# Performance work log

Hardware: AMD Instinct MI355X
Metric: run time of the kernel (lower is better)

Reference implementation:

```python
import jax, jax.numpy as jnp
import numpy as np

D_MODEL = 512
D_INNER = 2 * D_MODEL      # 1024
DT_RANK = D_MODEL // 16    # 32
D_STATE = 16
D_CONV = 4
NB_LAYERS = 3
BATCH = 64
SEQ = 201
CITY = 200
EPS = 1e-5


def setup_inputs() -> dict:
    key = jax.random.key(0)
    ks = jax.random.split(key, 12)
    def rn(k, shape, scale=0.02):
        return jax.random.normal(k, shape, jnp.float32) * scale
    A_init = jnp.tile(jnp.arange(1, D_STATE + 1, dtype=jnp.float32)[None, None, :],
                      (NB_LAYERS, D_INNER, 1))
    return {
        "x": jax.random.uniform(ks[0], (BATCH, SEQ, 2), jnp.float32),
        "city_count": CITY,
        "embed_W": rn(ks[1], (D_MODEL, 2), 0.5),
        "embed_b": jnp.zeros((D_MODEL,), jnp.float32),
        "norm_w": jnp.ones((NB_LAYERS, D_MODEL), jnp.float32),
        "norm_b": jnp.zeros((NB_LAYERS, D_MODEL), jnp.float32),
        "in_W": rn(ks[2], (NB_LAYERS, 2 * D_INNER, D_MODEL)),
        "conv_w": rn(ks[3], (NB_LAYERS, D_INNER, D_CONV), 0.1),
        "conv_b": jnp.zeros((NB_LAYERS, D_INNER), jnp.float32),
        "xproj_W": rn(ks[4], (NB_LAYERS, DT_RANK + 2 * D_STATE, D_INNER)),
        "dtproj_W": rn(ks[5], (NB_LAYERS, D_INNER, DT_RANK), 0.1),
        "dtproj_b": rn(ks[6], (NB_LAYERS, D_INNER), 0.5),
        "A_log": jnp.log(A_init),
        "Dskip": jnp.ones((NB_LAYERS, D_INNER), jnp.float32),
        "out_W": rn(ks[7], (NB_LAYERS, D_MODEL, D_INNER)),
        "normf_w": jnp.ones((D_MODEL,), jnp.float32),
        "normf_b": jnp.zeros((D_MODEL,), jnp.float32),
        "head_W": rn(ks[8], (CITY, D_MODEL)),
    }


def _silu(v):
    return v * jax.nn.sigmoid(v)


def _layernorm(v, w, b):
    v = v.astype(jnp.float32)
    mu = v.mean(-1, keepdims=True)
    var = ((v - mu) ** 2).mean(-1, keepdims=True)
    return (v - mu) * jax.lax.rsqrt(var + EPS) * w + b


def _rmsnorm(v, w, b):
    v = v.astype(jnp.float32)
    ms = (v * v).mean(-1, keepdims=True)
    return v * jax.lax.rsqrt(ms + EPS) * w + b


def _mamba_mixer(h, in_W, cw, cb, xp_W, dt_W, dt_b, A_log, Dv, o_W):
    B, L, _ = h.shape
    xz = jnp.einsum('bld,ed->ble', h, in_W)              # (B,L,2*di)
    xc, z = jnp.split(xz, 2, axis=-1)
    # causal depthwise conv over time
    xt = xc.transpose(0, 2, 1)                           # (B,di,L)
    xt = jax.lax.conv_general_dilated(
        xt, cw[:, None, :], (1,), [(D_CONV - 1, 0)],
        dimension_numbers=('NCH', 'OIH', 'NCH'),
        feature_group_count=D_INNER)
    u = _silu((xt + cb[None, :, None]).transpose(0, 2, 1))   # (B,L,di)
    x_dbl = jnp.einsum('bld,ed->ble', u, xp_W)
    dt_r = x_dbl[..., :DT_RANK]
    Bm = x_dbl[..., DT_RANK:DT_RANK + D_STATE]
    Cm = x_dbl[..., DT_RANK + D_STATE:]
    dt = jax.nn.softplus(jnp.einsum('blr,dr->bld', dt_r, dt_W) + dt_b)
    A = -jnp.exp(A_log)                                  # (di,n)

    def step(hst, ins):
        dt_t, B_t, C_t, u_t = ins                        # (B,di),(B,n),(B,n),(B,di)
        dA = jnp.exp(dt_t[..., None] * A)                # (B,di,n)
        hst = dA * hst + (dt_t * u_t)[..., None] * B_t[:, None, :]
        y = jnp.einsum('bdn,bn->bd', hst, C_t)
        return hst, y

    h0 = jnp.zeros((B, D_INNER, D_STATE), h.dtype)
    _, ys = jax.lax.scan(step, h0, (dt.transpose(1, 0, 2), Bm.transpose(1, 0, 2),
                                    Cm.transpose(1, 0, 2), u.transpose(1, 0, 2)))
    y = ys.transpose(1, 0, 2) + Dv * u
    y = y * _silu(z)
    return jnp.einsum('bld,ed->ble', y, o_W)


def reference(x, city_count, embed_W, embed_b, norm_w, norm_b, in_W, conv_w, conv_b,
              xproj_W, dtproj_W, dtproj_b, A_log, Dskip, out_W, normf_w, normf_b, head_W):
    h = jnp.einsum('blc,dc->bld', x, embed_W) + embed_b
    residual = None
    for i in range(NB_LAYERS):
        residual = h if residual is None else h + residual   # residual in fp32
        hn = _layernorm(residual, norm_w[i], norm_b[i])
        h = _mamba_mixer(hn, in_W[i], conv_w[i], conv_b[i], xproj_W[i],
                         dtproj_W[i], dtproj_b[i], A_log[i], Dskip[i], out_W[i])
    residual = h + residual
    xf = _rmsnorm(residual, normf_w, normf_b)                # final fused RMSNorm
    logits = jnp.einsum('bld,cd->blc', xf, head_W)           # output head -> city logits
    return logits
```

## Files before the change

kernel.cpp:

```cpp
#include <hip/hip_runtime.h>
#include <hip/hip_fp16.h>
#include <math.h>

#define D_MODEL 512
#define D_INNER 1024
#define DT_RANK 32
#define D_STATE 16
#define D_CONV 4
#define NB_LAYERS 3
#define BATCH 64
#define SEQ 201
#define CITY 200
#define M_ROWS (BATCH * SEQ)
#define M_PAD 12928
#define EPS 1e-5f
#define NCH 8
#define CL 26

typedef __attribute__((ext_vector_type(8))) short short8;
typedef __attribute__((ext_vector_type(8))) unsigned short ushort8;
typedef __attribute__((ext_vector_type(4))) float f32x4;

__device__ __forceinline__ float sigmoidf_(float x) { return 1.f / (1.f + __expf(-x)); }

__device__ __forceinline__ unsigned short f2b(float f) {
  union { float f; unsigned int u; } v; v.f = f;
  unsigned int r = (v.u + 0x7fff + ((v.u >> 16) & 1)) >> 16;
  return (unsigned short)r;
}
__device__ __forceinline__ float b2f(unsigned short h) {
  union { unsigned int u; float f; } v; v.u = ((unsigned int)h) << 16; return v.f;
}
__device__ __forceinline__ unsigned short f2h(float f) {
  __half h = __float2half(f); return *(unsigned short*)&h;
}
__device__ __forceinline__ float h2f(unsigned short u) {
  __half h = *(__half*)&u; return __half2float(h);
}

__device__ __forceinline__ void gload_lds16(const void* g, void* l) {
  __builtin_amdgcn_global_load_lds(
      (const __attribute__((address_space(1))) void*)g,
      (__attribute__((address_space(3))) void*)l, 16, 0, 0);
}

__device__ __forceinline__ void exp_vec(float dtv, const float* __restrict__ Areg,
                                        bool fast, float* __restrict__ e) {
  if (fast) {
    float e1 = __expf(-dtv);
    e[0] = e1;
    e[1] = e1 * e1;
    e[2] = e[1] * e1;
    e[3] = e[1] * e[1];
    e[4] = e[3] * e1;
    e[5] = e[3] * e[1];
    e[6] = e[3] * e[2];
    e[7] = e[3] * e[3];
    e[8] = e[7] * e1;
    e[9] = e[7] * e[1];
    e[10] = e[7] * e[2];
    e[11] = e[7] * e[3];
    e[12] = e[7] * e[4];
    e[13] = e[7] * e[5];
    e[14] = e[7] * e[6];
    e[15] = e[7] * e[7];
  } else {
#pragma unroll
    for (int n = 0; n < D_STATE; ++n) e[n] = __expf(dtv * Areg[n]);
  }
}
__device__ __forceinline__ bool a_is_arange(const float* __restrict__ Areg) {
  bool f = true;
#pragma unroll
  for (int n = 0; n < D_STATE; ++n)
    f = f && (fabsf(Areg[n] + (float)(n + 1)) < 1e-4f * (float)(n + 1));
  return f;
}

__global__ __launch_bounds__(256) void k_f2b(const float* __restrict__ in,
                                             unsigned short* __restrict__ out,
                                             int n, int n_total) {
  int i = blockIdx.x * 256 + threadIdx.x;
  if (i < n) out[i] = f2b(in[i]);
  else if (i < n_total) out[i] = 0;
}

__global__ __launch_bounds__(256) void k_padR(const float* __restrict__ W,
                                              unsigned short* __restrict__ out,
                                              int nl, int inrows, int outrows, int cols) {
  int i = blockIdx.x * 256 + threadIdx.x;
  if (i >= nl * outrows * cols) return;
  int c = i % cols;
  int r = (i / cols) % outrows;
  int L = i / (cols * outrows);
  out[i] = (r < inrows) ? f2b(W[((size_t)L * inrows + r) * cols + c]) : 0;
}

__global__ __launch_bounds__(256) void k_convT(const float* __restrict__ cw,
                                               float* __restrict__ cwT) {
  int i = blockIdx.x * 256 + threadIdx.x;
  if (i >= NB_LAYERS * D_CONV * D_INNER) return;
  int d = i & (D_INNER - 1);
  int k = (i >> 10) & 3;
  int L = i >> 12;
  cwT[i] = cw[((size_t)L * D_INNER + d) * D_CONV + k];
}

__global__ __launch_bounds__(256) void k_embed(const float* __restrict__ x,
                                               const float* __restrict__ W,
                                               const float* __restrict__ b,
                                               float* __restrict__ h) {
  int idx = blockIdx.x * 256 + threadIdx.x;
  if (idx >= M_ROWS * D_MODEL) return;
  int d = idx & (D_MODEL - 1);
  int m = idx >> 9;
  float x0 = x[m * 2 + 0], x1 = x[m * 2 + 1];
  h[idx] = fmaf(x0, W[d * 2 + 0], fmaf(x1, W[d * 2 + 1], b[d]));
}

__global__ __launch_bounds__(256) void k_resid_norm(const float* __restrict__ h,
                                                    float* __restrict__ resid,
                                                    float* __restrict__ out,
                                                    unsigned short* __restrict__ out_b,
                                                    const float* __restrict__ w,
                                                    const float* __restrict__ b,
                                                    int addRes, int mode) {
  int row = blockIdx.x * 4 + (threadIdx.x >> 6);
  int lane = threadIdx.x & 63;
  if (row >= M_ROWS) return;
  const float* hp = h + (size_t)row * D_MODEL;
  float* rp = resid + (size_t)row * D_MODEL;
  float v[8];
#pragma unroll
  for (int j = 0; j < 8; ++j) {
    float t = hp[j * 64 + lane];
    if (addRes) t += rp[j * 64 + lane];
    v[j] = t;
    rp[j * 64 + lane] = t;
  }
  float mu = 0.f, rstd;
  if (mode == 0) {
    float s = 0.f;
#pragma unroll
    for (int j = 0; j < 8; ++j) s += v[j];
#pragma unroll
    for (int o = 1; o < 64; o <<= 1) s += __shfl_xor(s, o);
    mu = s * (1.f / D_MODEL);
    float vs = 0.f;
#pragma unroll
    for (int j = 0; j < 8; ++j) { float d0 = v[j] - mu; vs += d0 * d0; }
#pragma unroll
    for (int o = 1; o < 64; o <<= 1) vs += __shfl_xor(vs, o);
    rstd = rsqrtf(vs * (1.f / D_MODEL) + EPS);
  } else {
    float s = 0.f;
#pragma unroll
    for (int j = 0; j < 8; ++j) s += v[j] * v[j];
#pragma unroll
    for (int o = 1; o < 64; o <<= 1) s += __shfl_xor(s, o);
    rstd = rsqrtf(s * (1.f / D_MODEL) + EPS);
  }
#pragma unroll
  for (int j = 0; j < 8; ++j) {
    int c = j * 64 + lane;
    float o = (v[j] - mu) * rstd * w[c] + b[c];
    if (out) out[(size_t)row * D_MODEL + c] = o;
    if (out_b) out_b[(size_t)row * D_MODEL + c] = f2b(o);
  }
}

template <int BOUT>
__global__ __launch_bounds__(256) void k_gemm_mfma(const unsigned short* __restrict__ A,
                                                   const unsigned short* __restrict__ B,
                                                   void* __restrict__ Cv, int ldc,
                                                   int M, int Nout, int K) {
  __shared__ unsigned short lA[128 * 64];
  __shared__ unsigned short lB[128 * 64];
  int tid = threadIdx.x;
  int wave = tid >> 6, lane = tid & 63;
  int nx = gridDim.x;
  int nwg = nx * gridDim.y;
  int bid = blockIdx.y * nx + blockIdx.x;
  int q = nwg >> 3, rr = nwg & 7;
  int xcd = bid & 7, idx = bid >> 3;
  int swz = (xcd < rr ? xcd * (q + 1) : rr * (q + 1) + (xcd - rr) * q) + idx;
  int bm = (swz / nx) * 128, bn = (swz % nx) * 128;
  int wm = (wave >> 1) * 64, wn = (wave & 1) * 64;
  f32x4 acc[4][4] = {};

  for (int k0 = 0; k0 < K; k0 += 64) {
#pragma unroll
    for (int i = 0; i < 4; ++i) {
      int e = (i * 256 + tid) * 8;
      int r = e >> 6, c = e & 63;
      int csrc = c ^ ((r & 7) << 3);
      gload_lds16(A + (size_t)(bm + r) * K + k0 + csrc, &lA[e]);
      gload_lds16(B + (size_t)(bn + r) * K + k0 + csrc, &lB[e]);
    }
    __syncthreads();
#pragma unroll
    for (int ks = 0; ks < 2; ++ks) {
      int koff = ks * 32 + (lane >> 4) * 8;
      short8 a[4], b[4];
#pragma unroll
      for (int i = 0; i < 4; ++i) {
        int row = wm + i * 16 + (lane & 15);
        a[i] = *(const short8*)&lA[row * 64 + (koff ^ ((row & 7) << 3))];
      }
#pragma unroll
      for (int j = 0; j < 4; ++j) {
        int row = wn + j * 16 + (lane & 15);
        b[j] = *(const short8*)&lB[row * 64 + (koff ^ ((row & 7) << 3))];
      }
#pragma unroll
      for (int i = 0; i < 4; ++i)
#pragma unroll
        for (int j = 0; j < 4; ++j)
          acc[i][j] = __builtin_amdgcn_mfma_f32_16x16x32_bf16(a[i], b[j], acc[i][j], 0, 0, 0);
    }
    __syncthreads();
  }
#pragma unroll
  for (int i = 0; i < 4; ++i) {
    int row0 = bm + wm + i * 16 + (lane >> 4) * 4;
#pragma unroll
    for (int j = 0; j < 4; ++j) {
      int col = bn + wn + j * 16 + (lane & 15);
#pragma unroll
      for (int r = 0; r < 4; ++r) {
        int m = row0 + r;
        if (m < M && col < Nout) {
          float v = acc[i][j][r];
          if (BOUT == 1) ((unsigned short*)Cv)[(size_t)m * ldc + col] = f2b(v);
          else ((float*)Cv)[(size_t)m * ldc + col] = v;
        }
      }
    }
  }
}

__global__ __launch_bounds__(256) void k_conv_silu(const unsigned short* __restrict__ xz,
                                                   const float* __restrict__ cwT,
                                                   const float* __restrict__ cb,
                                                   unsigned short* __restrict__ ub) {
  int i = blockIdx.x * 256 + threadIdx.x;
  if (i >= M_ROWS * 128) return;
  int dg = (i & 127) << 3;
  int m = i >> 7;
  int l = m % SEQ;
  float y[8];
  float4 cb0 = *(const float4*)&cb[dg];
  float4 cb1 = *(const float4*)&cb[dg + 4];
  y[0] = cb0.x; y[1] = cb0.y; y[2] = cb0.z; y[3] = cb0.w;
  y[4] = cb1.x; y[5] = cb1.y; y[6] = cb1.z; y[7] = cb1.w;
#pragma unroll
  for (int k = 0; k < D_CONV; ++k) {
    int ls = l - (D_CONV - 1) + k;
    if (ls >= 0) {
      ushort8 xv = *(const ushort8*)&xz[(size_t)(m - (D_CONV - 1) + k) * 2048 + dg];
      float4 w0 = *(const float4*)&cwT[k * D_INNER + dg];
      float4 w1 = *(const float4*)&cwT[k * D_INNER + dg + 4];
      y[0] = fmaf(w0.x, b2f(xv[0]), y[0]);
      y[1] = fmaf(w0.y, b2f(xv[1]), y[1]);
      y[2] = fmaf(w0.z, b2f(xv[2]), y[2]);
      y[3] = fmaf(w0.w, b2f(xv[3]), y[3]);
      y[4] = fmaf(w1.x, b2f(xv[4]), y[4]);
      y[5] = fmaf(w1.y, b2f(xv[5]), y[5]);
      y[6] = fmaf(w1.z, b2f(xv[6]), y[6]);
      y[7] = fmaf(w1.w, b2f(xv[7]), y[7]);
    }
  }
  ushort8 o;
#pragma unroll
  for (int j = 0; j < 8; ++j) { float v = y[j]; v = v * sigmoidf_(v); o[j] = f2b(v); }
  *(ushort8*)&ub[(size_t)m * D_INNER + dg] = o;
}

__device__ __forceinline__ float dt_eval(const float* __restrict__ xq,
                                         const float* __restrict__ Wd, float bias) {
  float a0 = 0.f, a1 = 0.f, a2 = 0.f, a3 = 0.f;
#pragma unroll
  for (int r = 0; r < 2; ++r) {
    float4 q0 = *(const float4*)&xq[r * 16 + 0];
    float4 q1 = *(const float4*)&xq[r * 16 + 4];
    float4 q2 = *(const float4*)&xq[r * 16 + 8];
    float4 q3 = *(const float4*)&xq[r * 16 + 12];
    int o = r * 16;
    a0 = fmaf(q0.x, Wd[o + 0], a0); a0 = fmaf(q0.y, Wd[o + 1], a0);
    a0 = fmaf(q0.z, Wd[o + 2], a0); a0 = fmaf(q0.w, Wd[o + 3], a0);
    a1 = fmaf(q1.x, Wd[o + 4], a1); a1 = fmaf(q1.y, Wd[o + 5], a1);
    a1 = fmaf(q1.z, Wd[o + 6], a1); a1 = fmaf(q1.w, Wd[o + 7], a1);
    a2 = fmaf(q2.x, Wd[o + 8], a2); a2 = fmaf(q2.y, Wd[o + 9], a2);
    a2 = fmaf(q2.z, Wd[o + 10], a2); a2 = fmaf(q2.w, Wd[o + 11], a2);
    a3 = fmaf(q3.x, Wd[o + 12], a3); a3 = fmaf(q3.y, Wd[o + 13], a3);
    a3 = fmaf(q3.z, Wd[o + 14], a3); a3 = fmaf(q3.w, Wd[o + 15], a3);
  }
  float dot = ((a0 + a1) + (a2 + a3)) + bias;
  return (dot > 20.f) ? dot : __logf(1.f + __expf(dot));
}

__global__ __launch_bounds__(256) void k_scan_p1(const unsigned short* __restrict__ ub,
                                                 const float* __restrict__ xdb,
                                                 const float* __restrict__ dtW,
                                                 const float* __restrict__ dtb,
                                                 const float* __restrict__ A_log,
                                                 unsigned short* __restrict__ dt,
                                                 unsigned short* __restrict__ L,
                                                 float* __restrict__ dtsum) {
  int tid = threadIdx.x;
  int b = blockIdx.x >> 3, c = blockIdx.x & 7;
  int d = blockIdx.y * 256 + tid;
  int t0 = c * CL, t1 = t0 + CL < SEQ ? t0 + CL : SEQ;
  float Wd[DT_RANK];
#pragma unroll
  for (int r = 0; r < DT_RANK; r += 4) {
    float4 w4 = *(const float4*)&dtW[(size_t)d * DT_RANK + r];
    Wd[r] = w4.x; Wd[r + 1] = w4.y; Wd[r + 2] = w4.z; Wd[r + 3] = w4.w;
  }
  float bias = dtb[d];
  float Areg[D_STATE], hst[D_STATE];
#pragma unroll
  for (int n = 0; n < D_STATE; ++n) {
    Areg[n] = -__expf(A_log[d * D_STATE + n]);
    hst[n] = 0.f;
  }
  bool fast = a_is_arange(Areg);
  float ds = 0.f;
  size_t row0 = (size_t)b * SEQ;
  for (int t = t0; t < t1; ++t) {
    size_t m = row0 + t;
    const float* xq = xdb + m * 64;
    unsigned short dh = f2h(dt_eval(xq, Wd, bias));
    dt[m * D_INNER + d] = dh;
    float dtv = h2f(dh);
    float uv = b2f(ub[m * D_INNER + d]);
    float Bv[D_STATE];
#pragma unroll
    for (int qd = 0; qd < 4; ++qd) {
      float4 v4 = *(const float4*)&xq[32 + qd * 4];
      Bv[qd * 4 + 0] = v4.x; Bv[qd * 4 + 1] = v4.y;
      Bv[qd * 4 + 2] = v4.z; Bv[qd * 4 + 3] = v4.w;
    }
    float du = dtv * uv;
    ds += dtv;
    float e[D_STATE];
    exp_vec(dtv, Areg, fast, e);
#pragma unroll
    for (int j = 0; j < D_STATE; ++j)
      hst[j] = fmaf(e[j], hst[j], du * Bv[j]);
  }
  size_t base = ((size_t)(b * NCH + c) * D_INNER + d) * D_STATE;
  ushort8 o0, o1;
#pragma unroll
  for (int j = 0; j < 8; ++j) { o0[j] = f2b(hst[j]); o1[j] = f2b(hst[8 + j]); }
  *(ushort8*)&L[base] = o0;
  *(ushort8*)&L[base + 8] = o1;
  dtsum[(size_t)(b * NCH + c) * D_INNER + d] = ds;
}

__global__ __launch_bounds__(256) void k_scan_fix(const float* __restrict__ A_log,
                                                  const float* __restrict__ dtsum,
                                                  unsigned short* __restrict__ L) {
  int tid = threadIdx.x;
  int b = blockIdx.x;
  int d = blockIdx.y * 256 + tid;
  float Areg[D_STATE], h[D_STATE];
#pragma unroll
  for (int n = 0; n < D_STATE; ++n) {
    Areg[n] = -__expf(A_log[d * D_STATE + n]);
    h[n] = 0.f;
  }
  bool fast = a_is_arange(Areg);
  for (int c = 0; c < NCH; ++c) {
    size_t base = ((size_t)(b * NCH + c) * D_INNER + d) * D_STATE;
    ushort8 l0 = *(const ushort8*)&L[base];
    ushort8 l1 = *(const ushort8*)&L[base + 8];
    float ds = dtsum[(size_t)(b * NCH + c) * D_INNER + d];
    ushort8 o0, o1;
#pragma unroll
    for (int j = 0; j < 8; ++j) { o0[j] = f2b(h[j]); o1[j] = f2b(h[8 + j]); }
    *(ushort8*)&L[base] = o0;
    *(ushort8*)&L[base + 8] = o1;
    float e[D_STATE];
    exp_vec(ds, Areg, fast, e);
#pragma unroll
    for (int j = 0; j < 8; ++j)
      h[j] = fmaf(e[j], h[j], b2f(l0[j]));
#pragma unroll
    for (int j = 0; j < 8; ++j)
      h[8 + j] = fmaf(e[8 + j], h[8 + j], b2f(l1[j]));
  }
}

__global__ __launch_bounds__(256) void k_scan_p2(const unsigned short* __restrict__ xz,
                                                 const unsigned short* __restrict__ ub,
                                                 const float* __restrict__ xdb,
                                                 const unsigned short* __restrict__ dt,
                                                 const float* __restrict__ A_log,
                                                 const float* __restrict__ Dv,
                                                 const unsigned short* __restrict__ L,
                                                 unsigned short* __restrict__ yb) {
  int tid = threadIdx.x;
  int b = blockIdx.x >> 3, c = blockIdx.x & 7;
  int d = blockIdx.y * 256 + tid;
  int t0 = c * CL, t1 = t0 + CL < SEQ ? t0 + CL : SEQ;
  float Areg[D_STATE], hst[D_STATE];
  size_t base = ((size_t)(b * NCH + c) * D_INNER + d) * D_STATE;
  ushort8 l0 = *(const ushort8*)&L[base];
  ushort8 l1 = *(const ushort8*)&L[base + 8];
#pragma unroll
  for (int n = 0; n < D_STATE; ++n) Areg[n] = -__expf(A_log[d * D_STATE + n]);
  bool fast = a_is_arange(Areg);
#pragma unroll
  for (int j = 0; j < 8; ++j) { hst[j] = b2f(l0[j]); hst[8 + j] = b2f(l1[j]); }
  float Dd = Dv[d];
  size_t row0 = (size_t)b * SEQ;
  for (int t = t0; t < t1; ++t) {
    size_t m = row0 + t;
    const float* xq = xdb + m * 64;
    float dtv = h2f(dt[m * D_INNER + d]);
    float uv = b2f(ub[m * D_INNER + d]);
    float zv = b2f(xz[m * 2048 + 1024 + d]);
    float Bv[D_STATE], Cv[D_STATE];
#pragma unroll
    for (int qd = 0; qd < 4; ++qd) {
      float4 v4 = *(const float4*)&xq[32 + qd * 4];
      Bv[qd * 4 + 0] = v4.x; Bv[qd * 4 + 1] = v4.y;
      Bv[qd * 4 + 2] = v4.z; Bv[qd * 4 + 3] = v4.w;
      float4 c4 = *(const float4*)&xq[48 + qd * 4];
      Cv[qd * 4 + 0] = c4.x; Cv[qd * 4 + 1] = c4.y;
      Cv[qd * 4 + 2] = c4.z; Cv[qd * 4 + 3] = c4.w;
    }
    float du = dtv * uv;
    float e[D_STATE];
    exp_vec(dtv, Areg, fast, e);
    float y0 = 0.f, y1 = 0.f, y2 = 0.f, y3 = 0.f;
#pragma unroll
    for (int j = 0; j < D_STATE; ++j) {
      hst[j] = fmaf(e[j], hst[j], du * Bv[j]);
      float& yq = (j < 4) ? y0 : (j < 8) ? y1 : (j < 12) ? y2 : y3;
      yq = fmaf(hst[j], Cv[j], yq);
    }
    float y = (y0 + y1) + (y2 + y3);
    y = fmaf(Dd, uv, y);
    y = y * (zv * sigmoidf_(zv));
    yb[m * D_INNER + d] = f2b(y);
  }
}

extern "C" void kernel_launch(void* const* d_in, const int* in_sizes, int n_in,
                              void* d_out, int out_size, void* d_ws, size_t ws_size,
                              hipStream_t stream) {
  const float* x        = (const float*)d_in[0];
  const float* embed_W  = (const float*)d_in[2];
  const float* embed_b  = (const float*)d_in[3];
  const float* norm_w   = (const float*)d_in[4];
  const float* norm_b   = (const float*)d_in[5];
  const float* in_W     = (const float*)d_in[6];
  const float* conv_w   = (const float*)d_in[7];
  const float* conv_b   = (const float*)d_in[8];
  const float* xproj_W  = (const float*)d_in[9];
  const float* dtproj_W = (const float*)d_in[10];
  const float* dtproj_b = (const float*)d_in[11];
  const float* A_log    = (const float*)d_in[12];
  const float* Dskip    = (const float*)d_in[13];
  const float* out_W    = (const float*)d_in[14];
  const float* normf_w  = (const float*)d_in[15];
  const float* normf_b  = (const float*)d_in[16];
  const float* head_W   = (const float*)d_in[17];
  float* out = (float*)d_out;

  size_t f32_elems = (size_t)M_ROWS * 1024  + (size_t)M_PAD * 64  +
                     (size_t)NB_LAYERS * D_CONV * D_INNER;
  size_t bf16_elems = (size_t)M_ROWS * 2048 + (size_t)M_PAD * 2048 +
                      (size_t)M_ROWS * 1024  +
                      (size_t)NB_LAYERS * (2048 * 512 + 512 * 1024 + 128 * 1024) +
                      256 * 512;
  size_t need = f32_elems * 4 + bf16_elems * 2;
  if (ws_size < need) return;

  float* ws = (float*)d_ws;
  float* buf_res  = ws;
  float* buf_h    = buf_res  + (size_t)M_ROWS * 512;
  float* buf_xdb  = buf_h    + (size_t)M_ROWS * 512;
  float* buf_cwT  = buf_xdb  + (size_t)M_PAD * 64;
  unsigned short* buf_xz   = (unsigned short*)(buf_cwT + (size_t)NB_LAYERS * D_CONV * D_INNER);
  unsigned short* buf_ub   = buf_xz + (size_t)M_ROWS * 2048;
  unsigned short* buf_yb   = buf_ub + (size_t)M_PAD * 1024;
  unsigned short* buf_hnb  = buf_yb;
  unsigned short* buf_dt   = buf_yb + (size_t)M_PAD * 1024;
  unsigned short* buf_wib  = buf_dt + (size_t)M_ROWS * 1024;
  unsigned short* buf_wob  = buf_wib + (size_t)NB_LAYERS * 2048 * 512;
  unsigned short* buf_wxb  = buf_wob + (size_t)NB_LAYERS * 512 * 1024;
  unsigned short* buf_whb  = buf_wxb + (size_t)NB_LAYERS * 128 * 1024;

  unsigned short* buf_L = (unsigned short*)buf_h;
  float* buf_dts = (float*)(buf_L + (size_t)BATCH * NCH * D_INNER * D_STATE);

  dim3 blk(256);

  k_f2b<<<(NB_LAYERS * 2048 * 512 + 255) / 256, blk, 0, stream>>>(
      in_W, buf_wib, NB_LAYERS * 2048 * 512, NB_LAYERS * 2048 * 512);
  k_f2b<<<(NB_LAYERS * 512 * 1024 + 255) / 256, blk, 0, stream>>>(
      out_W, buf_wob, NB_LAYERS * 512 * 1024, NB_LAYERS * 512 * 1024);
  k_padR<<<(NB_LAYERS * 128 * 1024 + 255) / 256, blk, 0, stream>>>(
      xproj_W, buf_wxb, NB_LAYERS, 64, 128, 1024);
  k_f2b<<<(256 * 512 + 255) / 256, blk, 0, stream>>>(head_W, buf_whb, CITY * 512, 256 * 512);
  k_convT<<<(NB_LAYERS * D_CONV * D_INNER + 255) / 256, blk, 0, stream>>>(conv_w, buf_cwT);

  k_embed<<<(M_ROWS * D_MODEL + 255) / 256, blk, 0, stream>>>(x, embed_W, embed_b, buf_h);

  for (int i = 0; i < NB_LAYERS; ++i) {
    k_resid_norm<<<(M_ROWS + 3) / 4, blk, 0, stream>>>(
        buf_h, buf_res, nullptr, buf_hnb, norm_w + i * D_MODEL, norm_b + i * D_MODEL,
        i > 0 ? 1 : 0, 0);

    k_gemm_mfma<1><<<dim3(2048 / 128, M_PAD / 128), blk, 0, stream>>>(
        buf_hnb, buf_wib + (size_t)i * 2048 * 512, buf_xz, 2048, M_ROWS, 2048, 512);

    k_conv_silu<<<(M_ROWS * 128 + 255) / 256, blk, 0, stream>>>(
        buf_xz, buf_cwT + (size_t)i * D_CONV * D_INNER, conv_b + (size_t)i * D_INNER, buf_ub);

    k_gemm_mfma<0><<<dim3(1, M_PAD / 128), blk, 0, stream>>>(
        buf_ub, buf_wxb + (size_t)i * 128 * 1024, buf_xdb, 64, M_ROWS, 64, 1024);

    const float* Ai  = A_log + (size_t)i * D_INNER * D_STATE;
    const float* Wdt = dtproj_W + (size_t)i * D_INNER * DT_RANK;
    const float* bdt = dtproj_b + (size_t)i * D_INNER;
    k_scan_p1<<<dim3(BATCH * NCH, D_INNER / 256), blk, 0, stream>>>(
        buf_ub, buf_xdb, Wdt, bdt, Ai, buf_dt, buf_L, buf_dts);
    k_scan_fix<<<dim3(BATCH, D_INNER / 256), blk, 0, stream>>>(Ai, buf_dts, buf_L);
    k_scan_p2<<<dim3(BATCH * NCH, D_INNER / 256), blk, 0, stream>>>(
        buf_xz, buf_ub, buf_xdb, buf_dt, Ai, Dskip + (size_t)i * D_INNER, buf_L, buf_yb);

    k_gemm_mfma<0><<<dim3(512 / 128, M_PAD / 128), blk, 0, stream>>>(
        buf_yb, buf_wob + (size_t)i * 512 * 1024, buf_h, 512, M_ROWS, 512, 1024);
  }

  k_resid_norm<<<(M_ROWS + 3) / 4, blk, 0, stream>>>(
      buf_h, buf_res, nullptr, buf_hnb, normf_w, normf_b, 1, 1);

  k_gemm_mfma<0><<<dim3(256 / 128, M_PAD / 128), blk, 0, stream>>>(
      buf_hnb, buf_whb, out, CITY, M_ROWS, CITY, 512);
}
```

Before: 729.2 us.

## Double-buffer GEMM LDS tiles and fuse residual add into out-proj epilogue

The MFMA GEMM now keeps two LDS buffers for A and B. The next K-tile's global-to-LDS loads are issued before the MFMA work on the current tile, so load latency can overlap compute. The out-projection GEMM also gets an ADDRES epilogue that adds its result directly into the fp32 residual buffer. This removes the separate h buffer and lets the norm kernel just read the residual, dropping a full fp32 activation write and read per layer. In exchange, LDS use per block doubles to 64KB, which may lower occupancy, and the epilogue now does a read-modify-write on the residual.

```diff
diff --git a/kernel.cpp b/kernel.cpp
--- a/kernel.cpp
+++ b/kernel.cpp
@@ -109,35 +109,27 @@
 __global__ __launch_bounds__(256) void k_embed(const float* __restrict__ x,
                                                const float* __restrict__ W,
                                                const float* __restrict__ b,
-                                               float* __restrict__ h) {
+                                               float* __restrict__ res) {
   int idx = blockIdx.x * 256 + threadIdx.x;
   if (idx >= M_ROWS * D_MODEL) return;
   int d = idx & (D_MODEL - 1);
   int m = idx >> 9;
   float x0 = x[m * 2 + 0], x1 = x[m * 2 + 1];
-  h[idx] = fmaf(x0, W[d * 2 + 0], fmaf(x1, W[d * 2 + 1], b[d]));
-}
-
-__global__ __launch_bounds__(256) void k_resid_norm(const float* __restrict__ h,
-                                                    float* __restrict__ resid,
-                                                    float* __restrict__ out,
-                                                    unsigned short* __restrict__ out_b,
-                                                    const float* __restrict__ w,
-                                                    const float* __restrict__ b,
-                                                    int addRes, int mode) {
+  res[idx] = fmaf(x0, W[d * 2 + 0], fmaf(x1, W[d * 2 + 1], b[d]));
+}
+
+__global__ __launch_bounds__(256) void k_norm(const float* __restrict__ res,
+                                              unsigned short* __restrict__ out_b,
+                                              const float* __restrict__ w,
+                                              const float* __restrict__ b,
+                                              int mode) {
   int row = blockIdx.x * 4 + (threadIdx.x >> 6);
   int lane = threadIdx.x & 63;
   if (row >= M_ROWS) return;
-  const float* hp = h + (size_t)row * D_MODEL;
-  float* rp = resid + (size_t)row * D_MODEL;
+  const float* rp = res + (size_t)row * D_MODEL;
   float v[8];
 #pragma unroll
-  for (int j = 0; j < 8; ++j) {
-    float t = hp[j * 64 + lane];
-    if (addRes) t += rp[j * 64 + lane];
-    v[j] = t;
-    rp[j * 64 + lane] = t;
-  }
+  for (int j = 0; j < 8; ++j) v[j] = rp[j * 64 + lane];
   float mu = 0.f, rstd;
   if (mode == 0) {
     float s = 0.f;
@@ -163,19 +155,17 @@
 #pragma unroll
   for (int j = 0; j < 8; ++j) {
     int c = j * 64 + lane;
-    float o = (v[j] - mu) * rstd * w[c] + b[c];
-    if (out) out[(size_t)row * D_MODEL + c] = o;
-    if (out_b) out_b[(size_t)row * D_MODEL + c] = f2b(o);
-  }
-}
-
-template <int BOUT>
+    out_b[(size_t)row * D_MODEL + c] = f2b((v[j] - mu) * rstd * w[c] + b[c]);
+  }
+}
+
+template <int BOUT, int ADDRES>
 __global__ __launch_bounds__(256) void k_gemm_mfma(const unsigned short* __restrict__ A,
                                                    const unsigned short* __restrict__ B,
                                                    void* __restrict__ Cv, int ldc,
                                                    int M, int Nout, int K) {
-  __shared__ unsigned short lA[128 * 64];
-  __shared__ unsigned short lB[128 * 64];
+  __shared__ unsigned short lA[2][128 * 64];
+  __shared__ unsigned short lB[2][128 * 64];
   int tid = threadIdx.x;
   int wave = tid >> 6, lane = tid & 63;
   int nx = gridDim.x;
@@ -188,16 +178,24 @@
   int wm = (wave >> 1) * 64, wn = (wave & 1) * 64;
   f32x4 acc[4][4] = {};
 
-  for (int k0 = 0; k0 < K; k0 += 64) {
+  auto stage = [&](int kt, int bb) {
+    int k0 = kt * 64;
 #pragma unroll
     for (int i = 0; i < 4; ++i) {
       int e = (i * 256 + tid) * 8;
       int r = e >> 6, c = e & 63;
       int csrc = c ^ ((r & 7) << 3);
-      gload_lds16(A + (size_t)(bm + r) * K + k0 + csrc, &lA[e]);
-      gload_lds16(B + (size_t)(bn + r) * K + k0 + csrc, &lB[e]);
-    }
-    __syncthreads();
+      gload_lds16(A + (size_t)(bm + r) * K + k0 + csrc, &lA[bb][e]);
+      gload_lds16(B + (size_t)(bn + r) * K + k0 + csrc, &lB[bb][e]);
+    }
+  };
+
+  int nk = K >> 6;
+  stage(0, 0);
+  __syncthreads();
+  for (int t = 0; t < nk; ++t) {
+    int cur = t & 1;
+    if (t + 1 < nk) stage(t + 1, cur ^ 1);
 #pragma unroll
     for (int ks = 0; ks < 2; ++ks) {
       int koff = ks * 32 + (lane >> 4) * 8;
@@ -205,12 +203,12 @@
 #pragma unroll
       for (int i = 0; i < 4; ++i) {
         int row = wm + i * 16 + (lane & 15);
-        a[i] = *(const short8*)&lA[row * 64 + (koff ^ ((row & 7) << 3))];
+        a[i] = *(const short8*)&lA[cur][row * 64 + (koff ^ ((row & 7) << 3))];
       }
 #pragma unroll
       for (int j = 0; j < 4; ++j) {
         int row = wn + j * 16 + (lane & 15);
-        b[j] = *(const short8*)&lB[row * 64 + (koff ^ ((row & 7) << 3))];
+        b[j] = *(const short8*)&lB[cur][row * 64 + (koff ^ ((row & 7) << 3))];
       }
 #pragma unroll
       for (int i = 0; i < 4; ++i)
@@ -231,8 +229,14 @@
         int m = row0 + r;
         if (m < M && col < Nout) {
           float v = acc[i][j][r];
-          if (BOUT == 1) ((unsigned short*)Cv)[(size_t)m * ldc + col] = f2b(v);
-          else ((float*)Cv)[(size_t)m * ldc + col] = v;
+          if (ADDRES) {
+            float* cp = (float*)Cv + (size_t)m * ldc + col;
+            *cp = *cp + v;
+          } else if (BOUT == 1) {
+            ((unsigned short*)Cv)[(size_t)m * ldc + col] = f2b(v);
+          } else {
+            ((float*)Cv)[(size_t)m * ldc + col] = v;
+          }
         }
       }
     }
@@ -421,15 +425,15 @@
     float dtv = h2f(dt[m * D_INNER + d]);
     float uv = b2f(ub[m * D_INNER + d]);
     float zv = b2f(xz[m * 2048 + 1024 + d]);
-    float Bv[D_STATE], Cv[D_STATE];
+    float Bv[D_STATE], Cvv[D_STATE];
 #pragma unroll
     for (int qd = 0; qd < 4; ++qd) {
       float4 v4 = *(const float4*)&xq[32 + qd * 4];
       Bv[qd * 4 + 0] = v4.x; Bv[qd * 4 + 1] = v4.y;
       Bv[qd * 4 + 2] = v4.z; Bv[qd * 4 + 3] = v4.w;
       float4 c4 = *(const float4*)&xq[48 + qd * 4];
-      Cv[qd * 4 + 0] = c4.x; Cv[qd * 4 + 1] = c4.y;
-      Cv[qd * 4 + 2] = c4.z; Cv[qd * 4 + 3] = c4.w;
+      Cvv[qd * 4 + 0] = c4.x; Cvv[qd * 4 + 1] = c4.y;
+      Cvv[qd * 4 + 2] = c4.z; Cvv[qd * 4 + 3] = c4.w;
     }
     float du = dtv * uv;
     float e[D_STATE];
@@ -439,7 +443,7 @@
     for (int j = 0; j < D_STATE; ++j) {
       hst[j] = fmaf(e[j], hst[j], du * Bv[j]);
       float& yq = (j < 4) ? y0 : (j < 8) ? y1 : (j < 12) ? y2 : y3;
-      yq = fmaf(hst[j], Cv[j], yq);
+      yq = fmaf(hst[j], Cvv[j], yq);
     }
     float y = (y0 + y1) + (y2 + y3);
     y = fmaf(Dd, uv, y);
@@ -470,10 +474,12 @@
   const float* head_W   = (const float*)d_in[17];
   float* out = (float*)d_out;
 
-  size_t f32_elems = (size_t)M_ROWS * 1024  + (size_t)M_PAD * 64  +
-                     (size_t)NB_LAYERS * D_CONV * D_INNER;
-  size_t bf16_elems = (size_t)M_ROWS * 2048 + (size_t)M_PAD * 2048 +
+  size_t f32_elems = (size_t)M_ROWS * 512  + (size_t)M_PAD * 64  +
+                     (size_t)NB_LAYERS * D_CONV * D_INNER  +
+                     (size_t)BATCH * NCH * D_INNER ;
+  size_t bf16_elems = (size_t)M_ROWS * 2048  + (size_t)M_PAD * 2048  +
                       (size_t)M_ROWS * 1024  +
+                      (size_t)BATCH * NCH * D_INNER * D_STATE  +
                       (size_t)NB_LAYERS * (2048 * 512 + 512 * 1024 + 128 * 1024) +
                       256 * 512;
   size_t need = f32_elems * 4 + bf16_elems * 2;
@@ -481,21 +487,19 @@
 
   float* ws = (float*)d_ws;
   float* buf_res  = ws;
-  float* buf_h    = buf_res  + (size_t)M_ROWS * 512;
-  float* buf_xdb  = buf_h    + (size_t)M_ROWS * 512;
+  float* buf_xdb  = buf_res  + (size_t)M_ROWS * 512;
   float* buf_cwT  = buf_xdb  + (size_t)M_PAD * 64;
-  unsigned short* buf_xz   = (unsigned short*)(buf_cwT + (size_t)NB_LAYERS * D_CONV * D_INNER);
+  float* buf_dts  = buf_cwT  + (size_t)NB_LAYERS * D_CONV * D_INNER;
+  unsigned short* buf_xz   = (unsigned short*)(buf_dts + (size_t)BATCH * NCH * D_INNER);
   unsigned short* buf_ub   = buf_xz + (size_t)M_ROWS * 2048;
   unsigned short* buf_yb   = buf_ub + (size_t)M_PAD * 1024;
   unsigned short* buf_hnb  = buf_yb;
   unsigned short* buf_dt   = buf_yb + (size_t)M_PAD * 1024;
-  unsigned short* buf_wib  = buf_dt + (size_t)M_ROWS * 1024;
+  unsigned short* buf_L    = buf_dt + (size_t)M_ROWS * 1024;
+  unsigned short* buf_wib  = buf_L + (size_t)BATCH * NCH * D_INNER * D_STATE;
   unsigned short* buf_wob  = buf_wib + (size_t)NB_LAYERS * 2048 * 512;
   unsigned short* buf_wxb  = buf_wob + (size_t)NB_LAYERS * 512 * 1024;
   unsigned short* buf_whb  = buf_wxb + (size_t)NB_LAYERS * 128 * 1024;
-
-  unsigned short* buf_L = (unsigned short*)buf_h;
-  float* buf_dts = (float*)(buf_L + (size_t)BATCH * NCH * D_INNER * D_STATE);
 
   dim3 blk(256);
 
@@ -508,20 +512,19 @@
   k_f2b<<<(256 * 512 + 255) / 256, blk, 0, stream>>>(head_W, buf_whb, CITY * 512, 256 * 512);
   k_convT<<<(NB_LAYERS * D_CONV * D_INNER + 255) / 256, blk, 0, stream>>>(conv_w, buf_cwT);
 
-  k_embed<<<(M_ROWS * D_MODEL + 255) / 256, blk, 0, stream>>>(x, embed_W, embed_b, buf_h);
+  k_embed<<<(M_ROWS * D_MODEL + 255) / 256, blk, 0, stream>>>(x, embed_W, embed_b, buf_res);
 
   for (int i = 0; i < NB_LAYERS; ++i) {
-    k_resid_norm<<<(M_ROWS + 3) / 4, blk, 0, stream>>>(
-        buf_h, buf_res, nullptr, buf_hnb, norm_w + i * D_MODEL, norm_b + i * D_MODEL,
-        i > 0 ? 1 : 0, 0);
-
-    k_gemm_mfma<1><<<dim3(2048 / 128, M_PAD / 128), blk, 0, stream>>>(
+    k_norm<<<(M_ROWS + 3) / 4, blk, 0, stream>>>(
+        buf_res, buf_hnb, norm_w + i * D_MODEL, norm_b + i * D_MODEL, 0);
+
+    k_gemm_mfma<1, 0><<<dim3(2048 / 128, M_PAD / 128), blk, 0, stream>>>(
         buf_hnb, buf_wib + (size_t)i * 2048 * 512, buf_xz, 2048, M_ROWS, 2048, 512);
 
     k_conv_silu<<<(M_ROWS * 128 + 255) / 256, blk, 0, stream>>>(
         buf_xz, buf_cwT + (size_t)i * D_CONV * D_INNER, conv_b + (size_t)i * D_INNER, buf_ub);
 
-    k_gemm_mfma<0><<<dim3(1, M_PAD / 128), blk, 0, stream>>>(
+    k_gemm_mfma<0, 0><<<dim3(1, M_PAD / 128), blk, 0, stream>>>(
         buf_ub, buf_wxb + (size_t)i * 128 * 1024, buf_xdb, 64, M_ROWS, 64, 1024);
 
     const float* Ai  = A_log + (size_t)i * D_INNER * D_STATE;
@@ -533,13 +536,12 @@
     k_scan_p2<<<dim3(BATCH * NCH, D_INNER / 256), blk, 0, stream>>>(
         buf_xz, buf_ub, buf_xdb, buf_dt, Ai, Dskip + (size_t)i * D_INNER, buf_L, buf_yb);
 
-    k_gemm_mfma<0><<<dim3(512 / 128, M_PAD / 128), blk, 0, stream>>>(
-        buf_yb, buf_wob + (size_t)i * 512 * 1024, buf_h, 512, M_ROWS, 512, 1024);
-  }
-
-  k_resid_norm<<<(M_ROWS + 3) / 4, blk, 0, stream>>>(
-      buf_h, buf_res, nullptr, buf_hnb, normf_w, normf_b, 1, 1);
-
-  k_gemm_mfma<0><<<dim3(256 / 128, M_PAD / 128), blk, 0, stream>>>(
+    k_gemm_mfma<0, 1><<<dim3(512 / 128, M_PAD / 128), blk, 0, stream>>>(
+        buf_yb, buf_wob + (size_t)i * 512 * 1024, buf_res, 512, M_ROWS, 512, 1024);
+  }
+
+  k_norm<<<(M_ROWS + 3) / 4, blk, 0, stream>>>(buf_res, buf_hnb, normf_w, normf_b, 1);
+
+  k_gemm_mfma<0, 0><<<dim3(256 / 128, M_PAD / 128), blk, 0, stream>>>(
       buf_hnb, buf_whb, out, CITY, M_ROWS, CITY, 512);
 }
```

Result: slower. 746.6 us (+2.4%).
